# Kernel optimization log

Measured on AMD Instinct MI355X. Metric: run time of the kernel, lower is better.

The kernel has to match this reference:

```python
import jax, jax.numpy as jnp
import numpy as np

CUTOFF = 5.0
MAX_NUM_PAIRS = 131072
N_ATOMS = 4096
BOX_L = 40.0


def setup_inputs() -> dict:
    key = jax.random.key(0)
    k1, _ = jax.random.split(key)
    positions = jax.random.uniform(k1, (N_ATOMS, 3), dtype=jnp.float32) * BOX_L
    box = jnp.eye(3, dtype=jnp.float32) * BOX_L  # triclinic box vectors (rows)
    return {"positions": positions, "box": box}


def _min_image_deltas(positions, box):
    # delta[i, j] = positions[i] - positions[j], wrapped by the minimum image
    # convention: subtract the nearest integer multiple of the box vectors.
    delta = positions[:, None, :] - positions[None, :, :]  # [N, N, 3]
    inv_box = jnp.linalg.inv(box)
    frac = delta @ inv_box                                  # fractional coords
    delta = delta - jnp.round(frac) @ box
    return delta


def reference(positions, box):
    n = positions.shape[0]
    delta = _min_image_deltas(positions, box)               # [N, N, 3]
    dist2 = jnp.sum(delta * delta, axis=-1)                 # [N, N]

    idx = jnp.arange(n)
    upper = idx[:, None] < idx[None, :]                     # unique pairs i<j
    mask = upper & (dist2 < CUTOFF * CUTOFF)

    n_pairs = jnp.sum(mask).astype(jnp.int32)
    # Compact hit pairs into a fixed-size buffer (static shape for jit).
    flat_idx, = jnp.nonzero(mask.ravel(), size=MAX_NUM_PAIRS, fill_value=0)
    valid = jnp.arange(MAX_NUM_PAIRS) < n_pairs

    pair_i = jnp.where(valid, flat_idx // n, -1)
    pair_j = jnp.where(valid, flat_idx % n, -1)
    pairs = jnp.stack([pair_i, pair_j], axis=0)             # [2, P]

    deltas = jnp.where(valid[:, None], delta.reshape(n * n, 3)[flat_idx], 0.0)
    d2 = jnp.where(valid, dist2.ravel()[flat_idx], 1.0)     # safe sqrt on pads
    distances = jnp.where(valid, jnp.sqrt(d2), 0.0)

    return pairs, deltas, distances, n_pairs
```

## Files before the change

### kernel.cpp

```cpp
#include <hip/hip_runtime.h>


#define CUT2 25.0f

__device__ __forceinline__ void load_box_inv(const float* __restrict__ box,
                                             float B[3][3], float Binv[3][3]) {
    #pragma unroll
    for (int r = 0; r < 3; ++r)
        #pragma unroll
        for (int c = 0; c < 3; ++c)
            B[r][c] = box[r * 3 + c];

    float a00 = B[0][0], a01 = B[0][1], a02 = B[0][2];
    float a10 = B[1][0], a11 = B[1][1], a12 = B[1][2];
    float a20 = B[2][0], a21 = B[2][1], a22 = B[2][2];

    float adj00 =  (a11 * a22 - a12 * a21);
    float adj01 = -(a01 * a22 - a02 * a21);
    float adj02 =  (a01 * a12 - a02 * a11);
    float adj10 = -(a10 * a22 - a12 * a20);
    float adj11 =  (a00 * a22 - a02 * a20);
    float adj12 = -(a00 * a12 - a02 * a10);
    float adj20 =  (a10 * a21 - a11 * a20);
    float adj21 = -(a00 * a21 - a01 * a20);
    float adj22 =  (a00 * a11 - a01 * a10);

    float det = a00 * adj00 + a01 * adj10 + a02 * adj20;

    Binv[0][0] = __fdiv_rn(adj00, det); Binv[0][1] = __fdiv_rn(adj01, det); Binv[0][2] = __fdiv_rn(adj02, det);
    Binv[1][0] = __fdiv_rn(adj10, det); Binv[1][1] = __fdiv_rn(adj11, det); Binv[1][2] = __fdiv_rn(adj12, det);
    Binv[2][0] = __fdiv_rn(adj20, det); Binv[2][1] = __fdiv_rn(adj21, det); Binv[2][2] = __fdiv_rn(adj22, det);
}

__device__ __forceinline__ void min_image(float xi, float yi, float zi,
                                          float xj, float yj, float zj,
                                          const float B[3][3], const float Binv[3][3],
                                          float& dx, float& dy, float& dz, float& d2) {
    dx = __fsub_rn(xi, xj);
    dy = __fsub_rn(yi, yj);
    dz = __fsub_rn(zi, zj);

    float f0 = __fadd_rn(__fadd_rn(__fmul_rn(dx, Binv[0][0]), __fmul_rn(dy, Binv[1][0])), __fmul_rn(dz, Binv[2][0]));
    float f1 = __fadd_rn(__fadd_rn(__fmul_rn(dx, Binv[0][1]), __fmul_rn(dy, Binv[1][1])), __fmul_rn(dz, Binv[2][1]));
    float f2 = __fadd_rn(__fadd_rn(__fmul_rn(dx, Binv[0][2]), __fmul_rn(dy, Binv[1][2])), __fmul_rn(dz, Binv[2][2]));

    float r0 = rintf(f0), r1 = rintf(f1), r2 = rintf(f2);

    float c0 = __fadd_rn(__fadd_rn(__fmul_rn(r0, B[0][0]), __fmul_rn(r1, B[1][0])), __fmul_rn(r2, B[2][0]));
    float c1 = __fadd_rn(__fadd_rn(__fmul_rn(r0, B[0][1]), __fmul_rn(r1, B[1][1])), __fmul_rn(r2, B[2][1]));
    float c2 = __fadd_rn(__fadd_rn(__fmul_rn(r0, B[0][2]), __fmul_rn(r1, B[1][2])), __fmul_rn(r2, B[2][2]));

    dx = __fsub_rn(dx, c0);
    dy = __fsub_rn(dy, c1);
    dz = __fsub_rn(dz, c2);

    d2 = __fadd_rn(__fadd_rn(__fmul_rn(dx, dx), __fmul_rn(dy, dy)), __fmul_rn(dz, dz));
}

__global__ void prep_kernel(const float* __restrict__ pos, float4* __restrict__ pos4,
                            float* __restrict__ out, int N, int P) {
    int idx = blockIdx.x * blockDim.x + threadIdx.x;
    int total = 6 * P + 1;
    for (int k = idx; k < total; k += gridDim.x * blockDim.x)
        out[k] = (k < 2 * P) ? -1.0f : 0.0f;
    if (idx < N)
        pos4[idx] = make_float4(pos[3 * idx], pos[3 * idx + 1], pos[3 * idx + 2], 0.0f);
}

__global__ void count_rows_kernel(const float4* __restrict__ pos4, const float* __restrict__ box,
                                  int* __restrict__ counts, unsigned long long* __restrict__ masks,
                                  int N) {
    int gwave = (blockIdx.x * blockDim.x + threadIdx.x) >> 6;
    int lane = threadIdx.x & 63;
    if (gwave >= N) return;
    int i = gwave;

    float B[3][3], Binv[3][3];
    load_box_inv(box, B, Binv);

    float4 pi = pos4[i];
    int nchunks = N >> 6;
    int c0 = i >> 6;
    unsigned long long* mrow = masks + (size_t)i * nchunks;

    int cnt = 0;

    {
        int j = (c0 << 6) + lane;
        bool hit = false;
        if (j > i) {
            float4 pj = pos4[j];
            float dx, dy, dz, d2;
            min_image(pi.x, pi.y, pi.z, pj.x, pj.y, pj.z, B, Binv, dx, dy, dz, d2);
            hit = (d2 < CUT2);
        }
        unsigned long long m = __ballot(hit);
        if (lane == 0) mrow[c0] = m;
        cnt += __popcll(m);
    }

    int c = c0 + 1;
    for (; c + 2 <= nchunks; c += 2) {
        int j0 = (c << 6) + lane;
        float4 pj0 = pos4[j0];
        float4 pj1 = pos4[j0 + 64];
        float dx0, dy0, dz0, d20, dx1, dy1, dz1, d21;
        min_image(pi.x, pi.y, pi.z, pj0.x, pj0.y, pj0.z, B, Binv, dx0, dy0, dz0, d20);
        min_image(pi.x, pi.y, pi.z, pj1.x, pj1.y, pj1.z, B, Binv, dx1, dy1, dz1, d21);
        unsigned long long m0 = __ballot(d20 < CUT2);
        unsigned long long m1 = __ballot(d21 < CUT2);
        if (lane == 0) { mrow[c] = m0; mrow[c + 1] = m1; }
        cnt += __popcll(m0) + __popcll(m1);
    }
    if (c < nchunks) {
        int j = (c << 6) + lane;
        float4 pj = pos4[j];
        float dx, dy, dz, d2;
        min_image(pi.x, pi.y, pi.z, pj.x, pj.y, pj.z, B, Binv, dx, dy, dz, d2);
        unsigned long long m = __ballot(d2 < CUT2);
        if (lane == 0) mrow[c] = m;
        cnt += __popcll(m);
    }

    if (lane == 0) counts[i] = cnt;
}

__global__ void scan_kernel(const int* __restrict__ counts, int* __restrict__ offsets,
                            float* __restrict__ out_npairs, int N) {
    int lane = threadIdx.x;
    int per = N >> 6;
    int base_idx = lane * per;

    int sum = 0;
    for (int r = 0; r < per; ++r) sum += counts[base_idx + r];

    int incl = sum;
    #pragma unroll
    for (int d = 1; d < 64; d <<= 1) {
        int t = __shfl_up(incl, d);
        if (lane >= d) incl += t;
    }
    int run = incl - sum;

    for (int r = 0; r < per; ++r) {
        int cv = counts[base_idx + r];
        offsets[base_idx + r] = run;
        run += cv;
    }
    if (lane == 63) *out_npairs = (float)incl;
}

__global__ void fill_rows_kernel(const float4* __restrict__ pos4, const float* __restrict__ box,
                                 const int* __restrict__ offsets,
                                 const unsigned long long* __restrict__ masks,
                                 float* __restrict__ out, int N, int P) {
    int gwave = (blockIdx.x * blockDim.x + threadIdx.x) >> 6;
    int lane = threadIdx.x & 63;
    if (gwave >= N) return;
    int i = gwave;

    int nchunks = N >> 6;
    int c0 = i >> 6;

    unsigned long long mymask = masks[(size_t)i * nchunks + lane];
    if (lane < c0) mymask = 0ull;

    float B[3][3], Binv[3][3];
    load_box_inv(box, B, Binv);
    float4 pi = pos4[i];

    int base = offsets[i];
    for (int c = c0; c < nchunks; ++c) {
        unsigned long long m = __shfl(mymask, c);
        if (m != 0ull) {
            bool hit = (m >> lane) & 1ull;
            if (hit) {
                int j = (c << 6) + lane;
                float4 pj = pos4[j];
                float dx, dy, dz, d2;
                min_image(pi.x, pi.y, pi.z, pj.x, pj.y, pj.z, B, Binv, dx, dy, dz, d2);
                int slot = base + __popcll(m & ((1ull << lane) - 1ull));
                if (slot < P) {
                    out[slot] = (float)i;
                    out[P + slot] = (float)j;
                    size_t db = 2 * (size_t)P + 3 * (size_t)slot;
                    out[db + 0] = dx;
                    out[db + 1] = dy;
                    out[db + 2] = dz;
                    out[5 * (size_t)P + slot] = sqrtf(d2);
                }
            }
            base += __popcll(m);
        }
    }
}

extern "C" void kernel_launch(void* const* d_in, const int* in_sizes, int n_in,
                              void* d_out, int out_size, void* d_ws, size_t ws_size,
                              hipStream_t stream) {
    const float* pos = (const float*)d_in[0];
    const float* box = (const float*)d_in[1];
    float* out = (float*)d_out;

    int N = in_sizes[0] / 3;
    int P = (out_size - 1) / 6;
    int nchunks = N >> 6;

    char* w = (char*)d_ws;
    int* counts = (int*)w;                         w += (size_t)N * sizeof(int);
    int* offsets = (int*)w;                        w += (size_t)N * sizeof(int);
    float4* pos4 = (float4*)w;                     w += (size_t)N * sizeof(float4);
    unsigned long long* masks = (unsigned long long*)w;

    int total_out = 6 * P + 1;
    int pad_blocks = (total_out + 255) / 256;
    prep_kernel<<<pad_blocks, 256, 0, stream>>>(pos, pos4, out, N, P);

    int row_threads = N * 64;
    int row_blocks = (row_threads + 255) / 256;
    count_rows_kernel<<<row_blocks, 256, 0, stream>>>(pos4, box, counts, masks, N);

    scan_kernel<<<1, 64, 0, stream>>>(counts, offsets, out + 6 * (size_t)P, N);

    fill_rows_kernel<<<row_blocks, 256, 0, stream>>>(pos4, box, offsets, masks, out, N, P);
}
```

Baseline: 101.2 us.

## Fuse neighbor-list stages into one cooperative kernel with grid sync

Replaces the four launches (prep, count, scan, fill) with a single cooperative kernel. Each wave keeps its row's chunk masks in registers instead of writing them to global memory, synchronises the whole grid once, then computes its own prefix offset by summing the earlier row counts. This removes launch overhead, the mask round trip and the serial single-wave scan. The cost is a redundant O(N) prefix sum per row, unpadded pos loads, and the requirement that all 1024 blocks be co-resident for the cooperative launch.

After: 203.2 us. 101% more time.

```diff
diff --git a/kernel.cpp b/kernel.cpp
--- a/kernel.cpp
+++ b/kernel.cpp
@@ -1,4 +1,7 @@
 #include <hip/hip_runtime.h>
+#include <hip/hip_cooperative_groups.h>
+
+namespace cg = cooperative_groups;
 
 
 #define CUT2 25.0f
@@ -57,128 +60,94 @@
     d2 = __fadd_rn(__fadd_rn(__fmul_rn(dx, dx), __fmul_rn(dy, dy)), __fmul_rn(dz, dz));
 }
 
-__global__ void prep_kernel(const float* __restrict__ pos, float4* __restrict__ pos4,
-                            float* __restrict__ out, int N, int P) {
-    int idx = blockIdx.x * blockDim.x + threadIdx.x;
+__global__ void __launch_bounds__(256, 4)
+nl_fused_kernel(const float* __restrict__ pos, const float* __restrict__ box,
+                float* __restrict__ out, int* __restrict__ counts, int N, int P) {
+    cg::grid_group grid = cg::this_grid();
+
+    int tid = blockIdx.x * blockDim.x + threadIdx.x;
+    int nthreads = gridDim.x * blockDim.x;
+    int i = tid >> 6;
+    int lane = tid & 63;
+    int nchunks = N >> 6;
+    int c0 = i >> 6;
+
     int total = 6 * P + 1;
-    for (int k = idx; k < total; k += gridDim.x * blockDim.x)
+    for (int k = tid; k < total; k += nthreads)
         out[k] = (k < 2 * P) ? -1.0f : 0.0f;
-    if (idx < N)
-        pos4[idx] = make_float4(pos[3 * idx], pos[3 * idx + 1], pos[3 * idx + 2], 0.0f);
-}
-
-__global__ void count_rows_kernel(const float4* __restrict__ pos4, const float* __restrict__ box,
-                                  int* __restrict__ counts, unsigned long long* __restrict__ masks,
-                                  int N) {
-    int gwave = (blockIdx.x * blockDim.x + threadIdx.x) >> 6;
-    int lane = threadIdx.x & 63;
-    if (gwave >= N) return;
-    int i = gwave;
 
     float B[3][3], Binv[3][3];
     load_box_inv(box, B, Binv);
 
-    float4 pi = pos4[i];
-    int nchunks = N >> 6;
-    int c0 = i >> 6;
-    unsigned long long* mrow = masks + (size_t)i * nchunks;
+    float xi = pos[3 * i + 0], yi = pos[3 * i + 1], zi = pos[3 * i + 2];
 
+    unsigned long long mymask = 0ull;
     int cnt = 0;
 
     {
         int j = (c0 << 6) + lane;
         bool hit = false;
         if (j > i) {
-            float4 pj = pos4[j];
             float dx, dy, dz, d2;
-            min_image(pi.x, pi.y, pi.z, pj.x, pj.y, pj.z, B, Binv, dx, dy, dz, d2);
+            min_image(xi, yi, zi, pos[3 * j + 0], pos[3 * j + 1], pos[3 * j + 2],
+                      B, Binv, dx, dy, dz, d2);
             hit = (d2 < CUT2);
         }
         unsigned long long m = __ballot(hit);
-        if (lane == 0) mrow[c0] = m;
+        if (lane == c0) mymask = m;
         cnt += __popcll(m);
     }
 
     int c = c0 + 1;
     for (; c + 2 <= nchunks; c += 2) {
         int j0 = (c << 6) + lane;
-        float4 pj0 = pos4[j0];
-        float4 pj1 = pos4[j0 + 64];
+        int j1 = j0 + 64;
         float dx0, dy0, dz0, d20, dx1, dy1, dz1, d21;
-        min_image(pi.x, pi.y, pi.z, pj0.x, pj0.y, pj0.z, B, Binv, dx0, dy0, dz0, d20);
-        min_image(pi.x, pi.y, pi.z, pj1.x, pj1.y, pj1.z, B, Binv, dx1, dy1, dz1, d21);
+        min_image(xi, yi, zi, pos[3 * j0 + 0], pos[3 * j0 + 1], pos[3 * j0 + 2],
+                  B, Binv, dx0, dy0, dz0, d20);
+        min_image(xi, yi, zi, pos[3 * j1 + 0], pos[3 * j1 + 1], pos[3 * j1 + 2],
+                  B, Binv, dx1, dy1, dz1, d21);
         unsigned long long m0 = __ballot(d20 < CUT2);
         unsigned long long m1 = __ballot(d21 < CUT2);
-        if (lane == 0) { mrow[c] = m0; mrow[c + 1] = m1; }
+        if (lane == c)     mymask = m0;
+        if (lane == c + 1) mymask = m1;
         cnt += __popcll(m0) + __popcll(m1);
     }
     if (c < nchunks) {
         int j = (c << 6) + lane;
-        float4 pj = pos4[j];
         float dx, dy, dz, d2;
-        min_image(pi.x, pi.y, pi.z, pj.x, pj.y, pj.z, B, Binv, dx, dy, dz, d2);
+        min_image(xi, yi, zi, pos[3 * j + 0], pos[3 * j + 1], pos[3 * j + 2],
+                  B, Binv, dx, dy, dz, d2);
         unsigned long long m = __ballot(d2 < CUT2);
-        if (lane == 0) mrow[c] = m;
+        if (lane == c) mymask = m;
         cnt += __popcll(m);
     }
 
     if (lane == 0) counts[i] = cnt;
-}
 
-__global__ void scan_kernel(const int* __restrict__ counts, int* __restrict__ offsets,
-                            float* __restrict__ out_npairs, int N) {
-    int lane = threadIdx.x;
-    int per = N >> 6;
-    int base_idx = lane * per;
+    grid.sync();
 
-    int sum = 0;
-    for (int r = 0; r < per; ++r) sum += counts[base_idx + r];
+    int pre = 0;
+    for (int b = 0; b < i; b += 64) {
+        int k = b + lane;
+        pre += (k < i) ? counts[k] : 0;
+    }
+    #pragma unroll
+    for (int d = 1; d < 64; d <<= 1)
+        pre += __shfl_xor(pre, d);
 
-    int incl = sum;
-    #pragma unroll
-    for (int d = 1; d < 64; d <<= 1) {
-        int t = __shfl_up(incl, d);
-        if (lane >= d) incl += t;
-    }
-    int run = incl - sum;
+    if (i == N - 1 && lane == 0)
+        out[6 * (size_t)P] = (float)(pre + cnt);
 
-    for (int r = 0; r < per; ++r) {
-        int cv = counts[base_idx + r];
-        offsets[base_idx + r] = run;
-        run += cv;
-    }
-    if (lane == 63) *out_npairs = (float)incl;
-}
-
-__global__ void fill_rows_kernel(const float4* __restrict__ pos4, const float* __restrict__ box,
-                                 const int* __restrict__ offsets,
-                                 const unsigned long long* __restrict__ masks,
-                                 float* __restrict__ out, int N, int P) {
-    int gwave = (blockIdx.x * blockDim.x + threadIdx.x) >> 6;
-    int lane = threadIdx.x & 63;
-    if (gwave >= N) return;
-    int i = gwave;
-
-    int nchunks = N >> 6;
-    int c0 = i >> 6;
-
-    unsigned long long mymask = masks[(size_t)i * nchunks + lane];
-    if (lane < c0) mymask = 0ull;
-
-    float B[3][3], Binv[3][3];
-    load_box_inv(box, B, Binv);
-    float4 pi = pos4[i];
-
-    int base = offsets[i];
-    for (int c = c0; c < nchunks; ++c) {
-        unsigned long long m = __shfl(mymask, c);
+    int base = pre;
+    for (int cc = c0; cc < nchunks; ++cc) {
+        unsigned long long m = __shfl(mymask, cc);
         if (m != 0ull) {
-            bool hit = (m >> lane) & 1ull;
-            if (hit) {
-                int j = (c << 6) + lane;
-                float4 pj = pos4[j];
+            if ((m >> lane) & 1ull) {
+                int j = (cc << 6) + lane;
                 float dx, dy, dz, d2;
-                min_image(pi.x, pi.y, pi.z, pj.x, pj.y, pj.z, B, Binv, dx, dy, dz, d2);
+                min_image(xi, yi, zi, pos[3 * j + 0], pos[3 * j + 1], pos[3 * j + 2],
+                          B, Binv, dx, dy, dz, d2);
                 int slot = base + __popcll(m & ((1ull << lane) - 1ull));
                 if (slot < P) {
                     out[slot] = (float)i;
@@ -204,23 +173,12 @@
 
     int N = in_sizes[0] / 3;
     int P = (out_size - 1) / 6;
-    int nchunks = N >> 6;
 
-    char* w = (char*)d_ws;
-    int* counts = (int*)w;                         w += (size_t)N * sizeof(int);
-    int* offsets = (int*)w;                        w += (size_t)N * sizeof(int);
-    float4* pos4 = (float4*)w;                     w += (size_t)N * sizeof(float4);
-    unsigned long long* masks = (unsigned long long*)w;
+    int* counts = (int*)d_ws;
 
-    int total_out = 6 * P + 1;
-    int pad_blocks = (total_out + 255) / 256;
-    prep_kernel<<<pad_blocks, 256, 0, stream>>>(pos, pos4, out, N, P);
-
-    int row_threads = N * 64;
-    int row_blocks = (row_threads + 255) / 256;
-    count_rows_kernel<<<row_blocks, 256, 0, stream>>>(pos4, box, counts, masks, N);
-
-    scan_kernel<<<1, 64, 0, stream>>>(counts, offsets, out + 6 * (size_t)P, N);
-
-    fill_rows_kernel<<<row_blocks, 256, 0, stream>>>(pos4, box, offsets, masks, out, N, P);
+    dim3 grid(N / 4), block(256);
+    void* args[] = {(void*)&pos, (void*)&box, (void*)&out, (void*)&counts,
+                    (void*)&N, (void*)&P};
+    hipLaunchCooperativeKernel((const void*)nl_fused_kernel, grid, block,
+                               args, 0, stream);
 }
```
